# Optimization experiments

Hardware: AMD Instinct MI355X
Metric: run time of the kernel (lower is better)

Reference implementation:

```python
import jax, jax.numpy as jnp
import numpy as np

N_AGENTS = 16      # args['num_agents']
BATCH = 8192       # args['n_rollout_threads'] -> number of independent graphs
OBS = 64           # cent_obs_shape[0] // n_nodes
HID = 128          # args['hidden_sizes'][0]
N_LAYERS = 2       # args['n_layers']
USE_RES = True     # args['use_res']


def _build_edges():
    # complete graph (no self loops) per graph, block-diagonal over BATCH graphs
    i, j = np.meshgrid(np.arange(N_AGENTS), np.arange(N_AGENTS), indexing='ij')
    m = i != j
    bs, bd = i[m], j[m]                      # [240]
    off = (np.arange(BATCH) * N_AGENTS)[:, None]
    src = (bs[None, :] + off).ravel().astype(np.int32)  # [BATCH*240]
    dst = (bd[None, :] + off).ravel().astype(np.int32)
    return src, dst


def setup_inputs() -> dict:
    key = jax.random.key(0)
    ks = jax.random.split(key, 5)
    N = BATCH * N_AGENTS
    src, dst = _build_edges()
    return {
        'cent_obs': jax.random.normal(ks[0], (N, OBS), jnp.float32),
        'w_emb': jax.random.normal(ks[1], (OBS, HID), jnp.float32) / np.sqrt(OBS).astype(np.float32),
        'b_emb': jnp.zeros((HID,), jnp.float32),
        'w_gcn': jax.random.normal(ks[2], (N_LAYERS, HID, HID), jnp.float32) / np.sqrt(HID).astype(np.float32),
        'b_gcn': jnp.zeros((N_LAYERS, HID), jnp.float32),
        'w_fc1': jax.random.normal(ks[3], (HID, 1), jnp.float32) / np.sqrt(HID).astype(np.float32),
        'b_fc1': jnp.zeros((1,), jnp.float32),
        'edge_src': jnp.asarray(src),
        'edge_dst': jnp.asarray(dst),
    }


def reference(cent_obs, w_emb, b_emb, w_gcn, b_gcn, w_fc1, b_fc1, edge_src, edge_dst):
    N = cent_obs.shape[0]
    # embedding_in
    x = cent_obs @ w_emb + b_emb                           # [N, HID]
    # GCNConv normalization with added self-loops (PyG default, sym norm)
    loop = jnp.arange(N, dtype=edge_src.dtype)
    src = jnp.concatenate([edge_src, loop])
    dst = jnp.concatenate([edge_dst, loop])
    deg = jax.ops.segment_sum(jnp.ones_like(dst, dtype=x.dtype), dst, num_segments=N)
    inv_sqrt = jax.lax.rsqrt(deg)
    norm = (inv_sqrt[src] * inv_sqrt[dst])[:, None]        # [E+N, 1]
    for l in range(N_LAYERS):
        h = x @ w_gcn[l]                                   # linear transform
        agg = jax.ops.segment_sum(h[src] * norm, dst, num_segments=N) + b_gcn[l]
        x = jnp.tanh(agg + x if USE_RES else agg)
    value = x @ w_fc1 + b_fc1                              # [N, 1]
    value = value.reshape(BATCH, -1)                       # [BATCH, n_nodes]
    return value.mean(axis=1).reshape(-1, 1)               # [BATCH, 1]
```

## Files before the change

### kernel.cpp

```cpp
#include <hip/hip_runtime.h>


#define N_GRAPHS 8192
#define BLOCK    256
#define NBLOCKS  (N_GRAPHS / 4)

typedef __attribute__((ext_vector_type(8))) short  short8;
typedef __attribute__((ext_vector_type(4))) float  floatx4;

#define MFMA16(a, b, c) __builtin_amdgcn_mfma_f32_16x16x32_bf16((a), (b), (c), 0, 0, 0)

__device__ __forceinline__ unsigned fbits(float x) {
  union { float f; unsigned u; } v; v.f = x; return v.u;
}
__device__ __forceinline__ float bitsf(unsigned u) {
  union { float f; unsigned u; } v; v.u = u; return v.f;
}
__device__ __forceinline__ void bsplit(float x, short& hi, short& lo) {
  unsigned hb = fbits(x) & 0xFFFF0000u;
  hi = (short)(hb >> 16);
  lo = (short)(fbits(x - bitsf(hb)) >> 16);
}
__device__ __forceinline__ float fast_tanh(float z) {
  float e = __expf(2.0f * z);
  return 1.0f - 2.0f / (e + 1.0f);
}

__device__ __forceinline__ void stage_w(const float* __restrict__ W, int kbase,
                                        short8* __restrict__ sHi,
                                        short8* __restrict__ sLo, int tid) {
  #pragma unroll
  for (int it = 0; it < 4; ++it) {
    int O  = it * 256 + tid;
    int cc = O & 15;
    int nt = (O >> 4) & 7;
    int qq = (O >> 7) & 3;
    int kc = (O >> 9) & 1;
    const float* src = W + (kbase + kc * 32 + qq * 8) * 128 + nt * 16 + cc;
    short8 hi, lo;
    #pragma unroll
    for (int j = 0; j < 8; ++j) {
      short h, l;
      bsplit(src[j * 128], h, l);
      hi[j] = h; lo[j] = l;
    }
    sHi[O] = hi;
    sLo[O] = lo;
  }
}

__global__ __launch_bounds__(BLOCK, 2) void gcn_mfma(
    const float* __restrict__ obs,
    const float* __restrict__ w_emb,
    const float* __restrict__ b_emb,
    const float* __restrict__ w_gcn,
    const float* __restrict__ b_gcn,
    const float* __restrict__ w_fc1,
    const float* __restrict__ b_fc1,
    float* __restrict__ out)
{
  __shared__ short8 sHi[1024];
  __shared__ short8 sLo[1024];
  __shared__ float  sM[4][128];

  const int tid = threadIdx.x;
  const int w   = tid >> 6;
  const int L   = tid & 63;
  const int q   = L >> 4;
  const int c   = L & 15;
  const int group = blockIdx.x * 4 + w;

  const float* orow = obs + (group * 16 + c) * 64 + q * 8;
  float4 o0 = *(const float4*)(orow);
  float4 o1 = *(const float4*)(orow + 4);
  float4 o2 = *(const float4*)(orow + 32);
  float4 o3 = *(const float4*)(orow + 36);

  stage_w(w_emb, 0, sHi, sLo, tid);
  __syncthreads();

  short8 a0h, a0l, a1h, a1l;
  {
    float t0[8] = {o0.x, o0.y, o0.z, o0.w, o1.x, o1.y, o1.z, o1.w};
    float t1[8] = {o2.x, o2.y, o2.z, o2.w, o3.x, o3.y, o3.z, o3.w};
    #pragma unroll
    for (int j = 0; j < 8; ++j) {
      short h, l;
      bsplit(t0[j], h, l); a0h[j] = h; a0l[j] = l;
      bsplit(t1[j], h, l); a1h[j] = h; a1l[j] = l;
    }
  }

  floatx4 x[8];
  #pragma unroll
  for (int nt = 0; nt < 8; ++nt) {
    float b = b_emb[nt * 16 + c];
    floatx4 acc = {b, b, b, b};
    int O = (q << 7) + (nt << 4) + c;
    short8 bh = sHi[O], bl = sLo[O];
    acc = MFMA16(a0h, bh, acc);
    acc = MFMA16(a0l, bh, acc);
    acc = MFMA16(a0h, bl, acc);
    bh = sHi[512 + O]; bl = sLo[512 + O];
    acc = MFMA16(a1h, bh, acc);
    acc = MFMA16(a1l, bh, acc);
    acc = MFMA16(a1h, bl, acc);
    x[nt] = acc;
  }

  #pragma unroll 1
  for (int l = 0; l < 2; ++l) {
    #pragma unroll
    for (int nt = 0; nt < 8; ++nt) {
      float s = x[nt][0] + x[nt][1] + x[nt][2] + x[nt][3];
      s += __shfl_xor(s, 16);
      s += __shfl_xor(s, 32);
      if (q == 0) sM[w][nt * 16 + c] = s * 0.0625f;
    }

    const float* wl = w_gcn + l * 16384;
    floatx4 h[8];
    #pragma unroll
    for (int nt = 0; nt < 8; ++nt) h[nt] = (floatx4){0.f, 0.f, 0.f, 0.f};

    #pragma unroll 1
    for (int half = 0; half < 2; ++half) {
      __syncthreads();
      stage_w(wl, half * 64, sHi, sLo, tid);
      __syncthreads();
      #pragma unroll
      for (int kc = 0; kc < 2; ++kc) {
        const float* mp = &sM[w][half * 64 + kc * 32 + q * 8];
        float4 m0 = *(const float4*)(mp);
        float4 m1 = *(const float4*)(mp + 4);
        float tm[8] = {m0.x, m0.y, m0.z, m0.w, m1.x, m1.y, m1.z, m1.w};
        short8 ah, al;
        #pragma unroll
        for (int j = 0; j < 8; ++j) {
          short hh, ll;
          bsplit(tm[j], hh, ll);
          ah[j] = hh; al[j] = ll;
        }
        #pragma unroll
        for (int nt = 0; nt < 8; ++nt) {
          int O = (kc << 9) + (q << 7) + (nt << 4) + c;
          short8 bh = sHi[O], bl = sLo[O];
          h[nt] = MFMA16(ah, bh, h[nt]);
          h[nt] = MFMA16(al, bh, h[nt]);
          h[nt] = MFMA16(ah, bl, h[nt]);
        }
      }
    }

    #pragma unroll
    for (int nt = 0; nt < 8; ++nt) {
      float hb = h[nt][0] + b_gcn[l * 128 + nt * 16 + c];
      x[nt][0] = fast_tanh(x[nt][0] + hb);
      x[nt][1] = fast_tanh(x[nt][1] + hb);
      x[nt][2] = fast_tanh(x[nt][2] + hb);
      x[nt][3] = fast_tanh(x[nt][3] + hb);
    }
  }

  float v = 0.f;
  #pragma unroll
  for (int nt = 0; nt < 8; ++nt)
    v += (x[nt][0] + x[nt][1] + x[nt][2] + x[nt][3]) * w_fc1[nt * 16 + c];
  v *= 0.0625f;
  v += __shfl_xor(v, 1);
  v += __shfl_xor(v, 2);
  v += __shfl_xor(v, 4);
  v += __shfl_xor(v, 8);
  v += __shfl_xor(v, 16);
  v += __shfl_xor(v, 32);
  if (L == 0) out[group] = v + b_fc1[0];
}

extern "C" void kernel_launch(void* const* d_in, const int* in_sizes, int n_in,
                              void* d_out, int out_size, void* d_ws, size_t ws_size,
                              hipStream_t stream) {
  const float* obs    = (const float*)d_in[0];
  const float* w_emb  = (const float*)d_in[1];
  const float* b_emb  = (const float*)d_in[2];
  const float* w_gcn  = (const float*)d_in[3];
  const float* b_gcn  = (const float*)d_in[4];
  const float* w_fc1  = (const float*)d_in[5];
  const float* b_fc1  = (const float*)d_in[6];
  float* out = (float*)d_out;

  gcn_mfma<<<NBLOCKS, BLOCK, 0, stream>>>(obs, w_emb, b_emb, w_gcn, b_gcn,
                                          w_fc1, b_fc1, out);
}
```

Measured before the change: 134.2 us.

## Pre-split weights into global bf16 fragment table and use 32x32 MFMA for embedding

A small prep kernel converts the embedding and GCN weights once per call into hi/lo bf16 MFMA fragment layouts in workspace. The main kernel then reads those fragments straight from global memory and cache instead of re-splitting and staging them through shared memory in every block. Each wave now handles two graphs using 32x32x16 MFMA for the embedding. The per-layer mean-feature GEMM is split across waves, with results exchanged through shared memory. This removes redundant per-block weight conversion and most barriers, but adds a second launch and uncoalesced-ish global fragment loads.

Measured after the change: 122.6 us. 8.6% less time.

```diff
diff --git a/kernel.cpp b/kernel.cpp
--- a/kernel.cpp
+++ b/kernel.cpp
@@ -3,12 +3,19 @@
 
 #define N_GRAPHS 8192
 #define BLOCK    256
-#define NBLOCKS  (N_GRAPHS / 4)
-
-typedef __attribute__((ext_vector_type(8))) short  short8;
-typedef __attribute__((ext_vector_type(4))) float  floatx4;
+#define NBLOCKS  (N_GRAPHS / 8)
+
+typedef __attribute__((ext_vector_type(8)))  short short8;
+typedef __attribute__((ext_vector_type(4)))  float floatx4;
+typedef __attribute__((ext_vector_type(16))) float floatx16;
 
 #define MFMA16(a, b, c) __builtin_amdgcn_mfma_f32_16x16x32_bf16((a), (b), (c), 0, 0, 0)
+#define MFMA32(a, b, c) __builtin_amdgcn_mfma_f32_32x32x16_bf16((a), (b), (c), 0, 0, 0)
+
+#define EMB_LO   1024
+#define GCN_BASE 2048
+#define GCN_LO   2048
+#define N_FRAGS  10240
 
 __device__ __forceinline__ unsigned fbits(float x) {
   union { float f; unsigned u; } v; v.f = x; return v.u;
@@ -26,154 +33,179 @@
   return 1.0f - 2.0f / (e + 1.0f);
 }
 
-__device__ __forceinline__ void stage_w(const float* __restrict__ W, int kbase,
-                                        short8* __restrict__ sHi,
-                                        short8* __restrict__ sLo, int tid) {
-  #pragma unroll
-  for (int it = 0; it < 4; ++it) {
-    int O  = it * 256 + tid;
-    int cc = O & 15;
-    int nt = (O >> 4) & 7;
-    int qq = (O >> 7) & 3;
-    int kc = (O >> 9) & 1;
-    const float* src = W + (kbase + kc * 32 + qq * 8) * 128 + nt * 16 + cc;
-    short8 hi, lo;
-    #pragma unroll
-    for (int j = 0; j < 8; ++j) {
-      short h, l;
-      bsplit(src[j * 128], h, l);
-      hi[j] = h; lo[j] = l;
-    }
-    sHi[O] = hi;
-    sLo[O] = lo;
-  }
-}
-
-__global__ __launch_bounds__(BLOCK, 2) void gcn_mfma(
+__global__ __launch_bounds__(BLOCK) void gcn_prep(
+    const float* __restrict__ w_emb, const float* __restrict__ w_gcn,
+    short8* __restrict__ ws)
+{
+  int f = blockIdx.x * BLOCK + threadIdx.x;
+  if (f >= 5120) return;
+  const float* src;
+  int hi_idx, lo_idx;
+  if (f < 1024) {
+    int ks = f >> 8, t = (f >> 6) & 3, L = f & 63;
+    int k0 = ks * 16 + (L >> 5) * 8;
+    int n  = t * 32 + (L & 31);
+    src = w_emb + k0 * 128 + n;
+    hi_idx = f; lo_idx = f + EMB_LO;
+  } else {
+    int f2 = f - 1024;
+    int l = f2 >> 11, r = f2 & 2047;
+    int kc = r >> 9, nt = (r >> 6) & 7, L = r & 63;
+    int k0 = kc * 32 + (L >> 4) * 8;
+    int n  = nt * 16 + (L & 15);
+    src = w_gcn + l * 16384 + k0 * 128 + n;
+    hi_idx = GCN_BASE + l * 4096 + r; lo_idx = hi_idx + GCN_LO;
+  }
+  short8 hi, lo;
+  #pragma unroll
+  for (int j = 0; j < 8; ++j) {
+    short h, l_;
+    bsplit(src[j * 128], h, l_);
+    hi[j] = h; lo[j] = l_;
+  }
+  ws[hi_idx] = hi;
+  ws[lo_idx] = lo;
+}
+
+__global__ __launch_bounds__(BLOCK, 4) void gcn_main(
     const float* __restrict__ obs,
-    const float* __restrict__ w_emb,
     const float* __restrict__ b_emb,
-    const float* __restrict__ w_gcn,
     const float* __restrict__ b_gcn,
     const float* __restrict__ w_fc1,
     const float* __restrict__ b_fc1,
+    const short8* __restrict__ tab,
     float* __restrict__ out)
 {
-  __shared__ short8 sHi[1024];
-  __shared__ short8 sLo[1024];
-  __shared__ float  sM[4][128];
+  __shared__ float sM[8][129];
+  __shared__ float sH[8][129];
 
   const int tid = threadIdx.x;
   const int w   = tid >> 6;
   const int L   = tid & 63;
+  const int m32 = L & 31;
+  const int kh  = L >> 5;
+  const int c16 = L & 15;
   const int q   = L >> 4;
-  const int c   = L & 15;
-  const int group = blockIdx.x * 4 + w;
-
-  const float* orow = obs + (group * 16 + c) * 64 + q * 8;
-  float4 o0 = *(const float4*)(orow);
-  float4 o1 = *(const float4*)(orow + 4);
-  float4 o2 = *(const float4*)(orow + 32);
-  float4 o3 = *(const float4*)(orow + 36);
-
-  stage_w(w_emb, 0, sHi, sLo, tid);
-  __syncthreads();
-
-  short8 a0h, a0l, a1h, a1l;
-  {
-    float t0[8] = {o0.x, o0.y, o0.z, o0.w, o1.x, o1.y, o1.z, o1.w};
-    float t1[8] = {o2.x, o2.y, o2.z, o2.w, o3.x, o3.y, o3.z, o3.w};
+  const int G0  = blockIdx.x * 8;
+  const int gw  = G0 + 2 * w;
+
+  const float* op = obs + (gw * 16 + m32) * 64 + kh * 8;
+  float4 ov[4][2];
+  #pragma unroll
+  for (int s = 0; s < 4; ++s) {
+    ov[s][0] = *(const float4*)(op + s * 16);
+    ov[s][1] = *(const float4*)(op + s * 16 + 4);
+  }
+
+  floatx16 x[4];
+  #pragma unroll
+  for (int t = 0; t < 4; ++t) {
+    float b = b_emb[t * 32 + m32];
+    #pragma unroll
+    for (int r = 0; r < 16; ++r) x[t][r] = b;
+  }
+  #pragma unroll
+  for (int s = 0; s < 4; ++s) {
+    float tmp[8] = {ov[s][0].x, ov[s][0].y, ov[s][0].z, ov[s][0].w,
+                    ov[s][1].x, ov[s][1].y, ov[s][1].z, ov[s][1].w};
+    short8 ah, al;
     #pragma unroll
     for (int j = 0; j < 8; ++j) {
-      short h, l;
-      bsplit(t0[j], h, l); a0h[j] = h; a0l[j] = l;
-      bsplit(t1[j], h, l); a1h[j] = h; a1l[j] = l;
-    }
-  }
-
-  floatx4 x[8];
-  #pragma unroll
-  for (int nt = 0; nt < 8; ++nt) {
-    float b = b_emb[nt * 16 + c];
-    floatx4 acc = {b, b, b, b};
-    int O = (q << 7) + (nt << 4) + c;
-    short8 bh = sHi[O], bl = sLo[O];
-    acc = MFMA16(a0h, bh, acc);
-    acc = MFMA16(a0l, bh, acc);
-    acc = MFMA16(a0h, bl, acc);
-    bh = sHi[512 + O]; bl = sLo[512 + O];
-    acc = MFMA16(a1h, bh, acc);
-    acc = MFMA16(a1l, bh, acc);
-    acc = MFMA16(a1h, bl, acc);
-    x[nt] = acc;
+      short h, l_;
+      bsplit(tmp[j], h, l_);
+      ah[j] = h; al[j] = l_;
+    }
+    #pragma unroll
+    for (int t = 0; t < 4; ++t) {
+      int idx = (s * 4 + t) * 64 + L;
+      short8 bh = tab[idx];
+      short8 bl = tab[idx + EMB_LO];
+      x[t] = MFMA32(ah, bh, x[t]);
+      x[t] = MFMA32(al, bh, x[t]);
+      x[t] = MFMA32(ah, bl, x[t]);
+    }
   }
 
   #pragma unroll 1
   for (int l = 0; l < 2; ++l) {
     #pragma unroll
-    for (int nt = 0; nt < 8; ++nt) {
-      float s = x[nt][0] + x[nt][1] + x[nt][2] + x[nt][3];
-      s += __shfl_xor(s, 16);
-      s += __shfl_xor(s, 32);
-      if (q == 0) sM[w][nt * 16 + c] = s * 0.0625f;
-    }
-
-    const float* wl = w_gcn + l * 16384;
-    floatx4 h[8];
-    #pragma unroll
-    for (int nt = 0; nt < 8; ++nt) h[nt] = (floatx4){0.f, 0.f, 0.f, 0.f};
-
-    #pragma unroll 1
-    for (int half = 0; half < 2; ++half) {
-      __syncthreads();
-      stage_w(wl, half * 64, sHi, sLo, tid);
-      __syncthreads();
-      #pragma unroll
-      for (int kc = 0; kc < 2; ++kc) {
-        const float* mp = &sM[w][half * 64 + kc * 32 + q * 8];
-        float4 m0 = *(const float4*)(mp);
-        float4 m1 = *(const float4*)(mp + 4);
-        float tm[8] = {m0.x, m0.y, m0.z, m0.w, m1.x, m1.y, m1.z, m1.w};
-        short8 ah, al;
-        #pragma unroll
-        for (int j = 0; j < 8; ++j) {
-          short hh, ll;
-          bsplit(tm[j], hh, ll);
-          ah[j] = hh; al[j] = ll;
-        }
-        #pragma unroll
-        for (int nt = 0; nt < 8; ++nt) {
-          int O = (kc << 9) + (q << 7) + (nt << 4) + c;
-          short8 bh = sHi[O], bl = sLo[O];
-          h[nt] = MFMA16(ah, bh, h[nt]);
-          h[nt] = MFMA16(al, bh, h[nt]);
-          h[nt] = MFMA16(ah, bl, h[nt]);
-        }
-      }
-    }
-
-    #pragma unroll
-    for (int nt = 0; nt < 8; ++nt) {
-      float hb = h[nt][0] + b_gcn[l * 128 + nt * 16 + c];
-      x[nt][0] = fast_tanh(x[nt][0] + hb);
-      x[nt][1] = fast_tanh(x[nt][1] + hb);
-      x[nt][2] = fast_tanh(x[nt][2] + hb);
-      x[nt][3] = fast_tanh(x[nt][3] + hb);
-    }
-  }
-
-  float v = 0.f;
-  #pragma unroll
-  for (int nt = 0; nt < 8; ++nt)
-    v += (x[nt][0] + x[nt][1] + x[nt][2] + x[nt][3]) * w_fc1[nt * 16 + c];
-  v *= 0.0625f;
-  v += __shfl_xor(v, 1);
-  v += __shfl_xor(v, 2);
-  v += __shfl_xor(v, 4);
-  v += __shfl_xor(v, 8);
-  v += __shfl_xor(v, 16);
-  v += __shfl_xor(v, 32);
-  if (L == 0) out[group] = v + b_fc1[0];
+    for (int t = 0; t < 4; ++t) {
+      float s0 = 0.f, s1 = 0.f;
+      #pragma unroll
+      for (int r = 0; r < 8; ++r) { s0 += x[t][r]; s1 += x[t][r + 8]; }
+      s0 += __shfl_xor(s0, 32);
+      s1 += __shfl_xor(s1, 32);
+      if (L < 32) {
+        sM[2 * w][t * 32 + L]     = s0 * 0.0625f;
+        sM[2 * w + 1][t * 32 + L] = s1 * 0.0625f;
+      }
+    }
+    __syncthreads();
+
+    floatx4 h0 = {0.f, 0.f, 0.f, 0.f};
+    floatx4 h1 = {0.f, 0.f, 0.f, 0.f};
+    #pragma unroll
+    for (int kc = 0; kc < 4; ++kc) {
+      short8 ah, al;
+      #pragma unroll
+      for (int j = 0; j < 8; ++j) {
+        int k = kc * 32 + q * 8 + j;
+        float mv = sM[c16 & 7][k];
+        if (c16 >= 8) mv = 0.f;
+        short h, l_;
+        bsplit(mv, h, l_);
+        ah[j] = h; al[j] = l_;
+      }
+      int base = GCN_BASE + l * 4096 + kc * 8 * 64 + L;
+      short8 bh0 = tab[base + (2 * w) * 64];
+      short8 bl0 = tab[base + (2 * w) * 64 + GCN_LO];
+      short8 bh1 = tab[base + (2 * w + 1) * 64];
+      short8 bl1 = tab[base + (2 * w + 1) * 64 + GCN_LO];
+      h0 = MFMA16(ah, bh0, h0); h0 = MFMA16(al, bh0, h0); h0 = MFMA16(ah, bl0, h0);
+      h1 = MFMA16(ah, bh1, h1); h1 = MFMA16(al, bh1, h1); h1 = MFMA16(ah, bl1, h1);
+    }
+    if (q < 2) {
+      #pragma unroll
+      for (int r = 0; r < 4; ++r) {
+        sH[q * 4 + r][(2 * w) * 16 + c16]     = h0[r];
+        sH[q * 4 + r][(2 * w + 1) * 16 + c16] = h1[r];
+      }
+    }
+    __syncthreads();
+
+    #pragma unroll
+    for (int t = 0; t < 4; ++t) {
+      float b  = b_gcn[l * 128 + t * 32 + m32];
+      float zA = sH[2 * w][t * 32 + m32] + b;
+      float zB = sH[2 * w + 1][t * 32 + m32] + b;
+      #pragma unroll
+      for (int r = 0; r < 8; ++r) {
+        x[t][r]     = fast_tanh(x[t][r] + zA);
+        x[t][r + 8] = fast_tanh(x[t][r + 8] + zB);
+      }
+    }
+  }
+
+  float vA = 0.f, vB = 0.f;
+  #pragma unroll
+  for (int t = 0; t < 4; ++t) {
+    float wf = w_fc1[t * 32 + m32];
+    float sA = 0.f, sB = 0.f;
+    #pragma unroll
+    for (int r = 0; r < 8; ++r) { sA += x[t][r]; sB += x[t][r + 8]; }
+    vA = fmaf(sA, wf, vA);
+    vB = fmaf(sB, wf, vB);
+  }
+  #pragma unroll
+  for (int d = 32; d >= 1; d >>= 1) {
+    vA += __shfl_xor(vA, d);
+    vB += __shfl_xor(vB, d);
+  }
+  if (L == 0) {
+    float bf = b_fc1[0];
+    out[gw]     = vA * 0.0625f + bf;
+    out[gw + 1] = vB * 0.0625f + bf;
+  }
 }
 
 extern "C" void kernel_launch(void* const* d_in, const int* in_sizes, int n_in,
@@ -187,7 +219,9 @@
   const float* w_fc1  = (const float*)d_in[5];
   const float* b_fc1  = (const float*)d_in[6];
   float* out = (float*)d_out;
-
-  gcn_mfma<<<NBLOCKS, BLOCK, 0, stream>>>(obs, w_emb, b_emb, w_gcn, b_gcn,
-                                          w_fc1, b_fc1, out);
-}
+  short8* tab = (short8*)d_ws;
+
+  gcn_prep<<<20, BLOCK, 0, stream>>>(w_emb, w_gcn, tab);
+  gcn_main<<<NBLOCKS, BLOCK, 0, stream>>>(obs, b_emb, b_gcn, w_fc1, b_fc1,
+                                          tab, out);
+}
```
